# Performance work log

Measured on AMD Instinct MI355X. Metric: run time of the kernel, lower is better.

## Reference

```python
import jax, jax.numpy as jnp
import numpy as np

B, N, D = 8, 4096, 512
NUM_CODES = 8192

def setup_inputs() -> dict:
    key = jax.random.key(0)
    kx, kc = jax.random.split(key)
    x = jax.random.normal(kx, (B, N, D), dtype=jnp.float32)
    codebook = jax.random.normal(kc, (NUM_CODES, D), dtype=jnp.float32)
    return {"x": x, "codebook": codebook}

def reference(x, codebook):
    # x: (B, N, D); codebook: (K, D)
    b = x.shape[0]
    flat = x.reshape(-1, x.shape[-1])  # (B*N, D)
    distances = (
        jnp.sum(flat * flat, axis=1, keepdims=True)
        + jnp.sum(codebook * codebook, axis=1)
        - 2.0 * flat @ codebook.T
    )
    codes = jnp.argmin(distances, axis=1).reshape(b, -1)  # (B, N) int
    return codes
```

## Files before the change

kernel.cpp:

```cpp
#include <hip/hip_runtime.h>
#include <hip/hip_bf16.h>
#include <hip/hip_fp16.h>


#define M_ROWS 32768
#define DDIM   512
#define KCODES 8192
#define NCAND  8

typedef unsigned long long u64;
typedef unsigned int u32;
typedef __attribute__((ext_vector_type(4))) float f32x4;
typedef __attribute__((ext_vector_type(8))) int v8i;

#define GL2LDS(gp, lp) __builtin_amdgcn_global_load_lds(                  \
    (const __attribute__((address_space(1))) void*)(gp),                  \
    (__attribute__((address_space(3))) void*)(lp), 16, 0, 0)

__device__ __forceinline__ u32 umin32(u32 a, u32 b) { return a < b ? a : b; }
__device__ __forceinline__ u32 umax32(u32 a, u32 b) { return a > b ? a : b; }
__device__ __forceinline__ u64 umin64(u64 a, u64 b) { return a < b ? a : b; }

__device__ __forceinline__ u32 fsort(float s) {
  u32 fb = __float_as_uint(s);
  return fb ^ (u32)(((int)fb >> 31) | 0x80000000);
}

__device__ __forceinline__ uint2 pk8_fp8(float4 v0, float4 v1) {
  int lo = 0, hi = 0;
  lo = __builtin_amdgcn_cvt_pk_fp8_f32(v0.x, v0.y, lo, false);
  lo = __builtin_amdgcn_cvt_pk_fp8_f32(v0.z, v0.w, lo, true);
  hi = __builtin_amdgcn_cvt_pk_fp8_f32(v1.x, v1.y, hi, false);
  hi = __builtin_amdgcn_cvt_pk_fp8_f32(v1.z, v1.w, hi, true);
  return (uint2){(u32)lo, (u32)hi};
}

__global__ __launch_bounds__(256) void conv_codebook_kernel(
    const float* __restrict__ cb, unsigned char* __restrict__ ch8,
    float* __restrict__ cnh) {
  int wave = (blockIdx.x * 256 + threadIdx.x) >> 6;
  int lane = threadIdx.x & 63;
  if (wave >= KCODES) return;
  const float* src = cb + (size_t)wave * DDIM + lane * 8;
  float4 v0 = *(const float4*)(src);
  float4 v1 = *(const float4*)(src + 4);
  *(uint2*)(ch8 + (size_t)wave * DDIM + lane * 8) = pk8_fp8(v0, v1);
  float ss = v0.x*v0.x + v0.y*v0.y + v0.z*v0.z + v0.w*v0.w
           + v1.x*v1.x + v1.y*v1.y + v1.z*v1.z + v1.w*v1.w;
#pragma unroll
  for (int off = 32; off; off >>= 1) ss += __shfl_xor(ss, off);
  if (lane == 0) cnh[wave] = 0.5f * ss;
}

__global__ __launch_bounds__(256) void conv_x_kernel(
    const float* __restrict__ x, unsigned char* __restrict__ xh8) {
  size_t i = ((size_t)blockIdx.x * 256 + threadIdx.x) * 8;
  float4 v0 = *(const float4*)(x + i);
  float4 v1 = *(const float4*)(x + i + 4);
  *(uint2*)(xh8 + i) = pk8_fp8(v0, v1);
}

__device__ __forceinline__ v8i ld_frag(const char* L, int row, int g) {
  const int base = row * 128;
  const int sl = ((g * 2) ^ (row & 7)) * 16;
  int4 lo = *(const int4*)&L[base + sl];
  int4 hi = *(const int4*)&L[base + (sl ^ 16)];
  v8i r;
  r[0] = lo.x; r[1] = lo.y; r[2] = lo.z; r[3] = lo.w;
  r[4] = hi.x; r[5] = hi.y; r[6] = hi.z; r[7] = hi.w;
  return r;
}

__global__ __launch_bounds__(256) void coarse_kernel(
    const unsigned char* __restrict__ xh8, const unsigned char* __restrict__ ch8,
    const float* __restrict__ cnh, uint4* __restrict__ part) {
  __shared__ __align__(16) char smem[34816];
  char* aL = smem;
  char* bL = smem + 16384;
  uint4* tab = (uint4*)smem;

  const int tid  = threadIdx.x;
  const int lane = tid & 63;
  const int wid  = tid >> 6;
  const int wm   = wid >> 1, wn = wid & 1;
  const int g    = lane >> 4, l16 = lane & 15;

  const int mblk = blockIdx.x & 255;
  const int nblk = blockIdx.x >> 8;
  const int row0 = mblk * 128;
  const int col0 = nblk * 128;

  const int a_ = lane >> 3, b_ = lane & 7;
  const size_t gsrc = (size_t)a_ * DDIM + ((b_ ^ a_) << 4);

  f32x4 acc[4][4];
#pragma unroll
  for (int tm = 0; tm < 4; ++tm)
#pragma unroll
    for (int tn = 0; tn < 4; ++tn) acc[tm][tn] = (f32x4){0.f, 0.f, 0.f, 0.f};

#pragma unroll
  for (int c = 0; c < 4; ++c) {
    __syncthreads();
#pragma unroll
    for (int j = 0; j < 4; ++j) {
      const int I = wid * 4 + j;
      const size_t off = (size_t)(I * 8) * DDIM + c * 128 + gsrc;
      GL2LDS(xh8 + (size_t)row0 * DDIM + off, aL + I * 1024);
      GL2LDS(ch8 + (size_t)col0 * DDIM + off, bL + I * 1024);
    }
    __syncthreads();

    v8i af[4];
#pragma unroll
    for (int t = 0; t < 4; ++t)
      af[t] = ld_frag(aL, wm * 64 + t * 16 + l16, g);
#pragma unroll
    for (int tn = 0; tn < 4; ++tn) {
      v8i bf = ld_frag(bL, wn * 64 + tn * 16 + l16, g);
#pragma unroll
      for (int tm = 0; tm < 4; ++tm)
        acc[tm][tn] = __builtin_amdgcn_mfma_scale_f32_16x16x128_f8f6f4(
            af[tm], bf, acc[tm][tn],
            0, 0,
            0, 0x7F7F7F7F,
            0, 0x7F7F7F7F);
    }
  }

  u32 codev[4];
  float cn[4];
#pragma unroll
  for (int tn = 0; tn < 4; ++tn) {
    codev[tn] = (u32)(col0 + wn * 64 + tn * 16 + l16);
    cn[tn] = cnh[codev[tn]];
  }

  u32 k1[16], k2[16], k3[16];
#pragma unroll
  for (int tm = 0; tm < 4; ++tm)
#pragma unroll
    for (int r = 0; r < 4; ++r) {
      const int sl = tm * 4 + r;
      k1[sl] = ~0u; k2[sl] = ~0u; k3[sl] = ~0u;
#pragma unroll
      for (int tn = 0; tn < 4; ++tn) {
        float s = cn[tn] - acc[tm][tn][r];
        u32 key = (__float_as_uint(s) & 0xFFFFE000u) | codev[tn];
        u32 t1 = umax32(k1[sl], key); k1[sl] = umin32(k1[sl], key);
        u32 t2 = umax32(k2[sl], t1);  k2[sl] = umin32(k2[sl], t1);
        k3[sl] = umin32(k3[sl], t2);
      }
    }

  u32 m1 = ~0u, m2 = ~0u, m3 = ~0u;
#pragma unroll
  for (int p = 0; p < 2; ++p) {
    __syncthreads();
    if (wn == p) {
#pragma unroll
      for (int tm = 0; tm < 4; ++tm)
#pragma unroll
        for (int r = 0; r < 4; ++r) {
          const int row = wm * 64 + tm * 16 + g * 4 + r;
          const int sl = tm * 4 + r;
          tab[row * 17 + l16] = (uint4){k1[sl], k2[sl], k3[sl], 0u};
        }
    }
    __syncthreads();
    if (tid < 128) {
#pragma unroll
      for (int e = 0; e < 16; ++e) {
        uint4 v = tab[tid * 17 + e];
        u32 t1 = umax32(m1, v.x); m1 = umin32(m1, v.x);
        u32 t2 = umax32(m2, t1);  m2 = umin32(m2, t1);
        m3 = umin32(m3, t2);
        t1 = umax32(m2, v.y);     m2 = umin32(m2, v.y);
        m3 = umin32(m3, t1);
        m3 = umin32(m3, v.z);
      }
    }
  }

  if (tid < 128)
    part[(size_t)nblk * M_ROWS + row0 + tid] = (uint4){m1, m2, m3, 0u};
}

__global__ __launch_bounds__(256) void merge_kernel(
    const uint4* __restrict__ part, int* __restrict__ cand) {
  const int row = blockIdx.x * 256 + threadIdx.x;
  u32 k[NCAND];
#pragma unroll
  for (int i = 0; i < NCAND; ++i) k[i] = ~0u;
  for (int nb = 0; nb < KCODES / 128; ++nb) {
    uint4 e = part[(size_t)nb * M_ROWS + row];
    u32 t = e.x;
#pragma unroll
    for (int i = 0; i < NCAND; ++i) { u32 mx = umax32(k[i], t); k[i] = umin32(k[i], t); t = mx; }
    t = e.y;
#pragma unroll
    for (int i = 0; i < NCAND; ++i) { u32 mx = umax32(k[i], t); k[i] = umin32(k[i], t); t = mx; }
    t = e.z;
#pragma unroll
    for (int i = 0; i < NCAND; ++i) { u32 mx = umax32(k[i], t); k[i] = umin32(k[i], t); t = mx; }
  }
#pragma unroll
  for (int i = 0; i < NCAND; ++i)
    cand[row * NCAND + i] = (int)(k[i] & 0x1FFFu);
}

__global__ __launch_bounds__(256) void rescore_kernel(
    const float* __restrict__ x, const float* __restrict__ cb,
    const float* __restrict__ cnh, const int* __restrict__ cand,
    int* __restrict__ out) {
  int wave = (blockIdx.x * 256 + threadIdx.x) >> 6;
  int lane = threadIdx.x & 63;
  if (wave >= M_ROWS) return;
  int idx[NCAND];
#pragma unroll
  for (int j = 0; j < NCAND; ++j) idx[j] = cand[wave * NCAND + j];

  const float* xr = x + (size_t)wave * DDIM + lane * 8;
  float4 x0 = *(const float4*)(xr);
  float4 x1 = *(const float4*)(xr + 4);

  float d[NCAND];
#pragma unroll
  for (int j = 0; j < NCAND; ++j) {
    const float* c = cb + (size_t)idx[j] * DDIM + lane * 8;
    float4 a0 = *(const float4*)(c);
    float4 a1 = *(const float4*)(c + 4);
    d[j] = x0.x*a0.x + x0.y*a0.y + x0.z*a0.z + x0.w*a0.w
         + x1.x*a1.x + x1.y*a1.y + x1.z*a1.z + x1.w*a1.w;
  }
#pragma unroll
  for (int off = 32; off; off >>= 1)
#pragma unroll
    for (int j = 0; j < NCAND; ++j) d[j] += __shfl_xor(d[j], off);

  if (lane == 0) {
    u64 best = ~0ull;
#pragma unroll
    for (int j = 0; j < NCAND; ++j) {
      float s = cnh[idx[j]] - d[j];
      u64 key = ((u64)fsort(s) << 32) | (u32)idx[j];
      best = umin64(best, key);
    }
    out[wave] = (int)(u32)best;
  }
}

extern "C" void kernel_launch(void* const* d_in, const int* in_sizes, int n_in,
                              void* d_out, int out_size, void* d_ws, size_t ws_size,
                              hipStream_t stream) {
  const float* x  = (const float*)d_in[0];
  const float* cb = (const float*)d_in[1];
  int* out = (int*)d_out;

  char* ws = (char*)d_ws;
  unsigned char* ch8  = (unsigned char*)(ws);
  unsigned char* xh8  = (unsigned char*)(ws + (size_t)4 * 1024 * 1024);
  float*         cnh  = (float*)(ws + (size_t)20 * 1024 * 1024);
  int*           cand = (int*)(ws + (size_t)20 * 1024 * 1024 + 32 * 1024);
  uint4*         part = (uint4*)(ws + (size_t)22 * 1024 * 1024);

  conv_codebook_kernel<<<KCODES / 4, 256, 0, stream>>>(cb, ch8, cnh);
  conv_x_kernel<<<(M_ROWS * DDIM) / (256 * 8), 256, 0, stream>>>(x, xh8);
  coarse_kernel<<<(M_ROWS / 128) * (KCODES / 128), 256, 0, stream>>>(xh8, ch8, cnh, part);
  merge_kernel<<<M_ROWS / 256, 256, 0, stream>>>(part, cand);
  rescore_kernel<<<M_ROWS / 4, 256, 0, stream>>>(x, cb, cnh, cand, out);
}
```

Measured before the change: 382.6 us.

## Double-buffer coarse kernel LDS tiles and use med3 for top-3 selection

The coarse kernel now prefetches the next 128-byte K-chunk into a second LDS buffer while MFMAs run on the current one, using 64 KB of shared memory instead of about 34 KB. This hides the global-to-LDS latency and drops one barrier per chunk. The top-3 candidate merge in registers and in the LDS reduction is rewritten with v_med3_u32 and three-way min, cutting the number of ALU ops. The codebook-norm loads are also hoisted before the main loop. The larger LDS footprint may lower occupancy, and the prefetch relies on the end-of-iteration barrier to keep the buffers from being overwritten while still in use.

```diff
diff --git a/kernel.cpp b/kernel.cpp
--- a/kernel.cpp
+++ b/kernel.cpp
@@ -20,6 +20,14 @@
 __device__ __forceinline__ u32 umin32(u32 a, u32 b) { return a < b ? a : b; }
 __device__ __forceinline__ u32 umax32(u32 a, u32 b) { return a > b ? a : b; }
 __device__ __forceinline__ u64 umin64(u64 a, u64 b) { return a < b ? a : b; }
+__device__ __forceinline__ u32 umin3(u32 a, u32 b, u32 c) {
+  return umin32(umin32(a, b), c);
+}
+__device__ __forceinline__ u32 med3u(u32 a, u32 b, u32 c) {
+  u32 d;
+  asm("v_med3_u32 %0, %1, %2, %3" : "=v"(d) : "v"(a), "v"(b), "v"(c));
+  return d;
+}
 
 __device__ __forceinline__ u32 fsort(float s) {
   u32 fb = __float_as_uint(s);
@@ -74,9 +82,7 @@
 __global__ __launch_bounds__(256) void coarse_kernel(
     const unsigned char* __restrict__ xh8, const unsigned char* __restrict__ ch8,
     const float* __restrict__ cnh, uint4* __restrict__ part) {
-  __shared__ __align__(16) char smem[34816];
-  char* aL = smem;
-  char* bL = smem + 16384;
+  __shared__ __align__(16) char smem[65536];
   uint4* tab = (uint4*)smem;
 
   const int tid  = threadIdx.x;
@@ -92,6 +98,27 @@
 
   const int a_ = lane >> 3, b_ = lane & 7;
   const size_t gsrc = (size_t)a_ * DDIM + ((b_ ^ a_) << 4);
+  const unsigned char* abase = xh8 + (size_t)row0 * DDIM + gsrc;
+  const unsigned char* bbase = ch8 + (size_t)col0 * DDIM + gsrc;
+
+#define STAGE(cc, buf) do {                                               \
+    char* sa_ = smem + (buf) * 32768;                                     \
+    _Pragma("unroll")                                                     \
+    for (int j = 0; j < 4; ++j) {                                         \
+      const int I_ = wid * 4 + j;                                         \
+      const size_t off_ = (size_t)(I_ * 8) * DDIM + (size_t)(cc) * 128;   \
+      GL2LDS(abase + off_, sa_ + I_ * 1024);                              \
+      GL2LDS(bbase + off_, sa_ + 16384 + I_ * 1024);                      \
+    }                                                                     \
+  } while (0)
+
+  u32 codev[4];
+  float cn[4];
+#pragma unroll
+  for (int tn = 0; tn < 4; ++tn) {
+    codev[tn] = (u32)(col0 + wn * 64 + tn * 16 + l16);
+    cn[tn] = cnh[codev[tn]];
+  }
 
   f32x4 acc[4][4];
 #pragma unroll
@@ -99,17 +126,14 @@
 #pragma unroll
     for (int tn = 0; tn < 4; ++tn) acc[tm][tn] = (f32x4){0.f, 0.f, 0.f, 0.f};
 
+  STAGE(0, 0);
+  __syncthreads();
+
 #pragma unroll
   for (int c = 0; c < 4; ++c) {
-    __syncthreads();
-#pragma unroll
-    for (int j = 0; j < 4; ++j) {
-      const int I = wid * 4 + j;
-      const size_t off = (size_t)(I * 8) * DDIM + c * 128 + gsrc;
-      GL2LDS(xh8 + (size_t)row0 * DDIM + off, aL + I * 1024);
-      GL2LDS(ch8 + (size_t)col0 * DDIM + off, bL + I * 1024);
-    }
-    __syncthreads();
+    if (c < 3) STAGE(c + 1, (c + 1) & 1);
+    const char* aL = smem + (c & 1) * 32768;
+    const char* bL = aL + 16384;
 
     v8i af[4];
 #pragma unroll
@@ -126,14 +150,7 @@
             0, 0x7F7F7F7F,
             0, 0x7F7F7F7F);
     }
-  }
-
-  u32 codev[4];
-  float cn[4];
-#pragma unroll
-  for (int tn = 0; tn < 4; ++tn) {
-    codev[tn] = (u32)(col0 + wn * 64 + tn * 16 + l16);
-    cn[tn] = cnh[codev[tn]];
+    __syncthreads();
   }
 
   u32 k1[16], k2[16], k3[16];
@@ -142,15 +159,24 @@
 #pragma unroll
     for (int r = 0; r < 4; ++r) {
       const int sl = tm * 4 + r;
-      k1[sl] = ~0u; k2[sl] = ~0u; k3[sl] = ~0u;
+      u32 key[4];
 #pragma unroll
       for (int tn = 0; tn < 4; ++tn) {
         float s = cn[tn] - acc[tm][tn][r];
-        u32 key = (__float_as_uint(s) & 0xFFFFE000u) | codev[tn];
-        u32 t1 = umax32(k1[sl], key); k1[sl] = umin32(k1[sl], key);
-        u32 t2 = umax32(k2[sl], t1);  k2[sl] = umin32(k2[sl], t1);
-        k3[sl] = umin32(k3[sl], t2);
+        key[tn] = (__float_as_uint(s) & 0xFFFFE000u) | codev[tn];
       }
+      u32 a1 = umin32(key[0], key[1]);
+      u32 a2 = umax32(key[0], key[1]);
+      u32 a3 = ~0u;
+      {
+        u32 lo = umin32(key[2], key[3]), hi = umax32(key[2], key[3]);
+        u32 m  = umax32(a1, lo);
+        a1 = umin32(a1, lo);
+        u32 b3 = med3u(a2, m, hi);
+        a2 = umin3(a2, m, hi);
+        a3 = umin32(a3, b3);
+      }
+      k1[sl] = a1; k2[sl] = a2; k3[sl] = a3;
     }
 
   u32 m1 = ~0u, m2 = ~0u, m3 = ~0u;
@@ -172,18 +198,18 @@
 #pragma unroll
       for (int e = 0; e < 16; ++e) {
         uint4 v = tab[tid * 17 + e];
-        u32 t1 = umax32(m1, v.x); m1 = umin32(m1, v.x);
-        u32 t2 = umax32(m2, t1);  m2 = umin32(m2, t1);
-        m3 = umin32(m3, t2);
-        t1 = umax32(m2, v.y);     m2 = umin32(m2, v.y);
-        m3 = umin32(m3, t1);
-        m3 = umin32(m3, v.z);
+        u32 a = umax32(m1, v.x);
+        m1 = umin32(m1, v.x);
+        u32 b = med3u(m2, a, v.y);
+        m2 = umin3(m2, a, v.y);
+        m3 = umin3(m3, b, v.z);
       }
     }
   }
 
   if (tid < 128)
     part[(size_t)nblk * M_ROWS + row0 + tid] = (uint4){m1, m2, m3, 0u};
+#undef STAGE
 }
 
 __global__ __launch_bounds__(256) void merge_kernel(
```

New measurement: 387.4 us. Within noise of the previous version (+1.3%).
